# Performance work log

Measured on AMD Instinct MI355X. Metric: run time of the kernel, lower is better.

The kernel has to match this reference:

```python
import jax, jax.numpy as jnp
import numpy as np

N_NODES = 100000
N_EDGES = 3200000
IN_CH = 512
HID = 16
OUT_CH = 2


def setup_inputs() -> dict:
    key = jax.random.key(0)
    k1, k2, k3, k4 = jax.random.split(key, 4)
    x = jax.random.normal(k1, (N_NODES, IN_CH), dtype=jnp.float32)
    edge_index = jax.random.randint(k2, (2, N_EDGES), 0, N_NODES, dtype=jnp.int32)
    # GCNConv weight (glorot-style scale) and zero bias; Linear xavier weight, zero bias
    W1 = jax.random.normal(k3, (IN_CH, HID), dtype=jnp.float32) * np.float32(np.sqrt(2.0 / (IN_CH + HID)))
    b1 = jnp.zeros((HID,), dtype=jnp.float32)
    W2 = jax.random.normal(k4, (HID, OUT_CH), dtype=jnp.float32) * np.float32(np.sqrt(2.0 / (HID + OUT_CH)))
    b2 = jnp.zeros((OUT_CH,), dtype=jnp.float32)
    return {"x": x, "edge_index": edge_index, "W1": W1, "b1": b1, "W2": W2, "b2": b2}


def reference(x, edge_index, W1, b1, W2, b2):
    # GCNConv with default add_self_loops=True, normalize=True:
    #   out = D^{-1/2} (A + I) D^{-1/2} X W1 + b1, then Linear(16, out).
    n = x.shape[0]
    loops = jnp.arange(n, dtype=edge_index.dtype)
    row = jnp.concatenate([edge_index[0], loops])  # source nodes j
    col = jnp.concatenate([edge_index[1], loops])  # target nodes i
    deg = jax.ops.segment_sum(jnp.ones_like(col, dtype=x.dtype), col, num_segments=n)
    dinv = jnp.where(deg > 0, jax.lax.rsqrt(deg), jnp.zeros_like(deg))
    norm = dinv[row] * dinv[col]  # [E+N]
    xw = x @ W1  # [N, 16] project first (PyG GCNConv order)
    agg = jax.ops.segment_sum(xw[row] * norm[:, None], col, num_segments=n)  # scatter-add to targets
    h = agg + b1
    return h @ W2 + b2  # [N, out_channels]
```

## Files before the change

### kernel.cpp

```cpp
#include <hip/hip_runtime.h>


constexpr int N_NODES = 100000;
constexpr int N_EDGES = 3200000;
constexpr int IN_CH   = 512;
constexpr int HID     = 16;
constexpr int OUT_CH  = 2;

constexpr int NBUCK      = (N_NODES + 255) / 256;
constexpr int BIN_BLOCKS = 320;
constexpr int EPB        = N_EDGES / BIN_BLOCKS;
constexpr int XW_BLOCKS  = (N_NODES + 63) / 64;

typedef __attribute__((ext_vector_type(4))) float floatx4;


__global__ __launch_bounds__(1024) void k_count_wc(const int* __restrict__ tgt,
                                                   int* __restrict__ hist,
                                                   const float* __restrict__ W1,
                                                   const float* __restrict__ b1,
                                                   const float* __restrict__ W2,
                                                   const float* __restrict__ b2,
                                                   float* __restrict__ Wc,
                                                   float* __restrict__ bconst) {
    if (blockIdx.x == BIN_BLOCKS) {
        for (int i = threadIdx.x; i < IN_CH * OUT_CH; i += 1024) {
            int c = i >> 1, o = i & 1;
            float s = 0.f;
#pragma unroll
            for (int h = 0; h < HID; ++h) s += W1[c * HID + h] * W2[h * OUT_CH + o];
            Wc[i] = s;
        }
        if (threadIdx.x < OUT_CH) {
            float bo = b2[threadIdx.x];
#pragma unroll
            for (int h = 0; h < HID; ++h) bo += b1[h] * W2[h * OUT_CH + threadIdx.x];
            bconst[threadIdx.x] = bo;
        }
        return;
    }
    __shared__ int h[NBUCK];
    for (int i = threadIdx.x; i < NBUCK; i += 1024) h[i] = 0;
    __syncthreads();
    int e0 = blockIdx.x * EPB;
    for (int e = e0 + threadIdx.x; e < e0 + EPB; e += 1024)
        atomicAdd(&h[tgt[e] >> 8], 1);
    __syncthreads();
    for (int i = threadIdx.x; i < NBUCK; i += 1024)
        hist[blockIdx.x * NBUCK + i] = h[i];
}

__global__ __launch_bounds__(64) void k_colscan(int* __restrict__ hist,
                                                int* __restrict__ coltot) {
    int b = blockIdx.x;
    int lane = threadIdx.x;
    int v[5];
    int s = 0;
#pragma unroll
    for (int j = 0; j < 5; ++j) {
        v[j] = hist[(lane * 5 + j) * NBUCK + b];
        s += v[j];
    }
    int inc = s;
#pragma unroll
    for (int off = 1; off < 64; off <<= 1) {
        int n = __shfl_up(inc, off);
        if (lane >= off) inc += n;
    }
    int excl = inc - s;
#pragma unroll
    for (int j = 0; j < 5; ++j) {
        hist[(lane * 5 + j) * NBUCK + b] = excl;
        excl += v[j];
    }
    if (lane == 63) coltot[b] = inc;
}

__global__ __launch_bounds__(512) void k_basescan(const int* __restrict__ coltot,
                                                  int* __restrict__ bbase) {
    __shared__ int tmp[512];
    int tid = threadIdx.x;
    int v = (tid < NBUCK) ? coltot[tid] : 0;
    tmp[tid] = v;
    __syncthreads();
#pragma unroll
    for (int off = 1; off < 512; off <<= 1) {
        int tv = (tid >= off) ? tmp[tid - off] : 0;
        __syncthreads();
        tmp[tid] += tv;
        __syncthreads();
    }
    if (tid < NBUCK) bbase[tid] = tmp[tid] - v;
    if (tid == NBUCK - 1) bbase[NBUCK] = tmp[tid];
}

__global__ __launch_bounds__(1024) void k_bin_xw(const int* __restrict__ ei,
                                                 const int* __restrict__ hist,
                                                 const int* __restrict__ coltot,
                                                 const int* __restrict__ bbase,
                                                 int* __restrict__ binned,
                                                 const float* __restrict__ x,
                                                 const float* __restrict__ Wc,
                                                 float2* __restrict__ t2) {
    if (blockIdx.x < BIN_BLOCKS) {
        __shared__ int goff[NBUCK];
        __shared__ int rlen[NBUCK];
        __shared__ int lofs[512];
        __shared__ int lcur[NBUCK];
        __shared__ int stage[EPB];
        int blk = blockIdx.x;
        int tid = threadIdx.x;
        for (int b = tid; b < NBUCK; b += 1024) {
            int g  = hist[blk * NBUCK + b];
            int nx = (blk == BIN_BLOCKS - 1) ? coltot[b]
                                             : hist[(blk + 1) * NBUCK + b];
            goff[b] = g;
            rlen[b] = nx - g;
        }
        __syncthreads();
        if (tid < 512) lofs[tid] = (tid < NBUCK) ? rlen[tid] : 0;
        __syncthreads();
#pragma unroll
        for (int off = 1; off < 512; off <<= 1) {
            int tv = 0;
            if (tid < 512 && tid >= off) tv = lofs[tid - off];
            __syncthreads();
            if (tid < 512) lofs[tid] += tv;
            __syncthreads();
        }
        for (int b = tid; b < NBUCK; b += 1024)
            lcur[b] = lofs[b] - rlen[b];
        __syncthreads();
        int e0 = blk * EPB;
        for (int e = e0 + tid; e < e0 + EPB; e += 1024) {
            int tg = ei[N_EDGES + e];
            int b = tg >> 8;
            int lpos = atomicAdd(&lcur[b], 1);
            stage[lpos] = ((tg & 255) << 20) | ei[e];
        }
        __syncthreads();
        int wv = tid >> 6, lane = tid & 63;
        for (int b = wv; b < NBUCK; b += 16) {
            int len = rlen[b];
            int gbase = bbase[b] + goff[b];
            int lbase = lofs[b] - len;
            for (int i = lane; i < len; i += 64)
                binned[gbase + i] = stage[lbase + i];
        }
        return;
    }
    int nb = blockIdx.x - BIN_BLOCKS;
    int wv = threadIdx.x >> 6;
    int lane = threadIdx.x & 63;
    int node = nb * 64 + wv * 4;
    int r0 = min(node,     N_NODES - 1);
    int r1 = min(node + 1, N_NODES - 1);
    int r2 = min(node + 2, N_NODES - 1);
    int r3 = min(node + 3, N_NODES - 1);
    const floatx4* x0 = reinterpret_cast<const floatx4*>(x + (size_t)r0 * IN_CH + lane * 8);
    const floatx4* x1 = reinterpret_cast<const floatx4*>(x + (size_t)r1 * IN_CH + lane * 8);
    const floatx4* x2 = reinterpret_cast<const floatx4*>(x + (size_t)r2 * IN_CH + lane * 8);
    const floatx4* x3 = reinterpret_cast<const floatx4*>(x + (size_t)r3 * IN_CH + lane * 8);
    const floatx4* wr = reinterpret_cast<const floatx4*>(Wc + lane * 16);
    floatx4 a0 = x0[0], a1 = x0[1];
    floatx4 b0 = x1[0], b1 = x1[1];
    floatx4 c0 = x2[0], c1 = x2[1];
    floatx4 d0 = x3[0], d1 = x3[1];
    floatx4 w0 = wr[0], w1 = wr[1], w2 = wr[2], w3 = wr[3];
    float s0x = a0[0]*w0[0] + a0[1]*w0[2] + a0[2]*w1[0] + a0[3]*w1[2]
              + a1[0]*w2[0] + a1[1]*w2[2] + a1[2]*w3[0] + a1[3]*w3[2];
    float s0y = a0[0]*w0[1] + a0[1]*w0[3] + a0[2]*w1[1] + a0[3]*w1[3]
              + a1[0]*w2[1] + a1[1]*w2[3] + a1[2]*w3[1] + a1[3]*w3[3];
    float s1x = b0[0]*w0[0] + b0[1]*w0[2] + b0[2]*w1[0] + b0[3]*w1[2]
              + b1[0]*w2[0] + b1[1]*w2[2] + b1[2]*w3[0] + b1[3]*w3[2];
    float s1y = b0[0]*w0[1] + b0[1]*w0[3] + b0[2]*w1[1] + b0[3]*w1[3]
              + b1[0]*w2[1] + b1[1]*w2[3] + b1[2]*w3[1] + b1[3]*w3[3];
    float s2x = c0[0]*w0[0] + c0[1]*w0[2] + c0[2]*w1[0] + c0[3]*w1[2]
              + c1[0]*w2[0] + c1[1]*w2[2] + c1[2]*w3[0] + c1[3]*w3[2];
    float s2y = c0[0]*w0[1] + c0[1]*w0[3] + c0[2]*w1[1] + c0[3]*w1[3]
              + c1[0]*w2[1] + c1[1]*w2[3] + c1[2]*w3[1] + c1[3]*w3[3];
    float s3x = d0[0]*w0[0] + d0[1]*w0[2] + d0[2]*w1[0] + d0[3]*w1[2]
              + d1[0]*w2[0] + d1[1]*w2[2] + d1[2]*w3[0] + d1[3]*w3[2];
    float s3y = d0[0]*w0[1] + d0[1]*w0[3] + d0[2]*w1[1] + d0[3]*w1[3]
              + d1[0]*w2[1] + d1[1]*w2[3] + d1[2]*w3[1] + d1[3]*w3[3];
#pragma unroll
    for (int off = 32; off; off >>= 1) {
        s0x += __shfl_xor(s0x, off); s0y += __shfl_xor(s0y, off);
        s1x += __shfl_xor(s1x, off); s1y += __shfl_xor(s1y, off);
        s2x += __shfl_xor(s2x, off); s2y += __shfl_xor(s2y, off);
        s3x += __shfl_xor(s3x, off); s3y += __shfl_xor(s3y, off);
    }
    if (node + lane < N_NODES) {
        if      (lane == 0) t2[node]     = make_float2(s0x, s0y);
        else if (lane == 1) t2[node + 1] = make_float2(s1x, s1y);
        else if (lane == 2) t2[node + 2] = make_float2(s2x, s2y);
        else if (lane == 3) t2[node + 3] = make_float2(s3x, s3y);
    }
}

__global__ __launch_bounds__(1024) void k_dinv(const int* __restrict__ bbase,
                                               const int* __restrict__ binned,
                                               float* __restrict__ dinv,
                                               float2* __restrict__ t2) {
    __shared__ int cnt[256];
    if (threadIdx.x < 256) cnt[threadIdx.x] = 0;
    __syncthreads();
    int b = blockIdx.x;
    int s = bbase[b], e = bbase[b + 1];
    for (int i = s + threadIdx.x; i < e; i += 1024)
        atomicAdd(&cnt[binned[i] >> 20], 1);
    __syncthreads();
    if (threadIdx.x < 256) {
        int node = (b << 8) + threadIdx.x;
        if (node < N_NODES) {
            float di = rsqrtf((float)(cnt[threadIdx.x] + 1));
            dinv[node] = di;
            float2 v = t2[node];
            t2[node] = make_float2(v.x * di, v.y * di);
        }
    }
}

__global__ __launch_bounds__(1024) void k_acc(const int* __restrict__ bbase,
                                              const int* __restrict__ binned,
                                              const float2* __restrict__ t2,
                                              const float* __restrict__ dinv,
                                              const float* __restrict__ bconst,
                                              float2* __restrict__ out) {
    __shared__ float acc0[256];
    __shared__ float acc1[256];
    if (threadIdx.x < 256) {
        acc0[threadIdx.x] = 0.f;
        acc1[threadIdx.x] = 0.f;
    }
    __syncthreads();
    int b = blockIdx.x;
    int s = bbase[b], e = bbase[b + 1];
    for (int i = s + threadIdx.x; i < e; i += 1024) {
        int v = binned[i];
        float2 ts = t2[v & 0xFFFFF];
        atomicAdd(&acc0[v >> 20], ts.x);
        atomicAdd(&acc1[v >> 20], ts.y);
    }
    __syncthreads();
    if (threadIdx.x < 256) {
        int node = (b << 8) + threadIdx.x;
        if (node < N_NODES) {
            float2 self = t2[node];
            float di = dinv[node];
            out[node] = make_float2(di * (acc0[threadIdx.x] + self.x) + bconst[0],
                                    di * (acc1[threadIdx.x] + self.y) + bconst[1]);
        }
    }
}

extern "C" void kernel_launch(void* const* d_in, const int* in_sizes, int n_in,
                              void* d_out, int out_size, void* d_ws, size_t ws_size,
                              hipStream_t stream) {
    const float* x  = (const float*)d_in[0];
    const int*   ei = (const int*)d_in[1];
    const float* W1 = (const float*)d_in[2];
    const float* b1 = (const float*)d_in[3];
    const float* W2 = (const float*)d_in[4];
    const float* b2 = (const float*)d_in[5];

    char* ws = (char*)d_ws;
    int*    hist   = (int*)   (ws + 0);
    int*    coltot = (int*)   (ws + 500480);
    int*    bbase  = (int*)   (ws + 502048);
    float*  Wc     = (float*) (ws + 503616);
    float*  bconst = (float*) (ws + 507712);
    float*  dinv   = (float*) (ws + 507728);
    float2* t2     = (float2*)(ws + 907728);
    int*    binned = (int*)   (ws + 1707728);

    k_count_wc<<<BIN_BLOCKS + 1, 1024, 0, stream>>>(ei + N_EDGES, hist,
                                                    W1, b1, W2, b2, Wc, bconst);
    k_colscan <<<NBUCK, 64, 0, stream>>>(hist, coltot);
    k_basescan<<<1, 512, 0, stream>>>(coltot, bbase);
    k_bin_xw  <<<BIN_BLOCKS + XW_BLOCKS, 1024, 0, stream>>>(ei, hist, coltot,
                                                            bbase, binned,
                                                            x, Wc, t2);
    k_dinv    <<<NBUCK, 1024, 0, stream>>>(bbase, binned, dinv, t2);
    k_acc     <<<NBUCK, 1024, 0, stream>>>(bbase, binned, t2, dinv, bconst,
                                           (float2*)d_out);
}
```

Baseline: 371.4 us.

## Fuse all stages into one cooperative persistent kernel with grid syncs

Replaces the six separate kernel launches (count, column scan, base scan, bin+xw, dinv, accumulate) with a single cooperative kernel whose persistent blocks loop over virtual blocks and separate stages with grid.sync. The edge-count partitioning also changes from 320 to 512 virtual blocks, which shrinks the per-block staging buffer to fit a shared 8192-int scratch array, and the copy-out uses 16-lane groups instead of full wavefronts. The aim is to remove launch gaps and tail effects between stages. The cost is fixed grid size (at most 512 blocks, limited by occupancy), grid-wide barrier overhead, and larger per-block loops.

```diff
diff --git a/kernel.cpp b/kernel.cpp
--- a/kernel.cpp
+++ b/kernel.cpp
@@ -1,4 +1,7 @@
 #include <hip/hip_runtime.h>
+#include <hip/hip_cooperative_groups.h>
+
+namespace cg = cooperative_groups;
 
 
 constexpr int N_NODES = 100000;
@@ -7,258 +10,245 @@
 constexpr int HID     = 16;
 constexpr int OUT_CH  = 2;
 
-constexpr int NBUCK      = (N_NODES + 255) / 256;
-constexpr int BIN_BLOCKS = 320;
-constexpr int EPB        = N_EDGES / BIN_BLOCKS;
-constexpr int XW_BLOCKS  = (N_NODES + 63) / 64;
+constexpr int NBUCK  = (N_NODES + 255) / 256;
+constexpr int CNT_VB = 512;
+constexpr int EPB    = N_EDGES / CNT_VB;
+constexpr int XW_VB  = (N_NODES + 63) / 64;
 
 typedef __attribute__((ext_vector_type(4))) float floatx4;
 
 
-__global__ __launch_bounds__(1024) void k_count_wc(const int* __restrict__ tgt,
-                                                   int* __restrict__ hist,
-                                                   const float* __restrict__ W1,
-                                                   const float* __restrict__ b1,
-                                                   const float* __restrict__ W2,
-                                                   const float* __restrict__ b2,
-                                                   float* __restrict__ Wc,
-                                                   float* __restrict__ bconst) {
-    if (blockIdx.x == BIN_BLOCKS) {
-        for (int i = threadIdx.x; i < IN_CH * OUT_CH; i += 1024) {
+__global__ __launch_bounds__(1024) void k_mega(const int* __restrict__ ei,
+                                               const float* __restrict__ x,
+                                               const float* __restrict__ W1,
+                                               const float* __restrict__ b1,
+                                               const float* __restrict__ W2,
+                                               const float* __restrict__ b2,
+                                               int* __restrict__ hist,
+                                               int* __restrict__ coltot,
+                                               int* __restrict__ bbase,
+                                               float* __restrict__ Wc,
+                                               float* __restrict__ bconst,
+                                               float* __restrict__ dinv,
+                                               float2* __restrict__ t2,
+                                               int* __restrict__ binned,
+                                               float2* __restrict__ out) {
+    __shared__ int smem[8192];
+    cg::grid_group grid = cg::this_grid();
+    const int tid = threadIdx.x;
+    const int G = gridDim.x;
+    const int* tgt = ei + N_EDGES;
+
+    for (int v = blockIdx.x; v < CNT_VB; v += G) {
+        for (int i = tid; i < NBUCK; i += 1024) smem[i] = 0;
+        __syncthreads();
+        int e0 = v * EPB;
+        for (int e = e0 + tid; e < e0 + EPB; e += 1024)
+            atomicAdd(&smem[tgt[e] >> 8], 1);
+        __syncthreads();
+        for (int i = tid; i < NBUCK; i += 1024)
+            hist[v * NBUCK + i] = smem[i];
+        __syncthreads();
+    }
+    if (blockIdx.x == 0) {
+        for (int i = tid; i < IN_CH * OUT_CH; i += 1024) {
             int c = i >> 1, o = i & 1;
             float s = 0.f;
 #pragma unroll
             for (int h = 0; h < HID; ++h) s += W1[c * HID + h] * W2[h * OUT_CH + o];
             Wc[i] = s;
         }
-        if (threadIdx.x < OUT_CH) {
-            float bo = b2[threadIdx.x];
-#pragma unroll
-            for (int h = 0; h < HID; ++h) bo += b1[h] * W2[h * OUT_CH + threadIdx.x];
-            bconst[threadIdx.x] = bo;
-        }
-        return;
-    }
-    __shared__ int h[NBUCK];
-    for (int i = threadIdx.x; i < NBUCK; i += 1024) h[i] = 0;
-    __syncthreads();
-    int e0 = blockIdx.x * EPB;
-    for (int e = e0 + threadIdx.x; e < e0 + EPB; e += 1024)
-        atomicAdd(&h[tgt[e] >> 8], 1);
-    __syncthreads();
-    for (int i = threadIdx.x; i < NBUCK; i += 1024)
-        hist[blockIdx.x * NBUCK + i] = h[i];
-}
-
-__global__ __launch_bounds__(64) void k_colscan(int* __restrict__ hist,
-                                                int* __restrict__ coltot) {
-    int b = blockIdx.x;
-    int lane = threadIdx.x;
-    int v[5];
-    int s = 0;
-#pragma unroll
-    for (int j = 0; j < 5; ++j) {
-        v[j] = hist[(lane * 5 + j) * NBUCK + b];
-        s += v[j];
-    }
-    int inc = s;
-#pragma unroll
-    for (int off = 1; off < 64; off <<= 1) {
-        int n = __shfl_up(inc, off);
-        if (lane >= off) inc += n;
-    }
-    int excl = inc - s;
-#pragma unroll
-    for (int j = 0; j < 5; ++j) {
-        hist[(lane * 5 + j) * NBUCK + b] = excl;
-        excl += v[j];
-    }
-    if (lane == 63) coltot[b] = inc;
-}
-
-__global__ __launch_bounds__(512) void k_basescan(const int* __restrict__ coltot,
-                                                  int* __restrict__ bbase) {
-    __shared__ int tmp[512];
-    int tid = threadIdx.x;
-    int v = (tid < NBUCK) ? coltot[tid] : 0;
-    tmp[tid] = v;
-    __syncthreads();
-#pragma unroll
-    for (int off = 1; off < 512; off <<= 1) {
-        int tv = (tid >= off) ? tmp[tid - off] : 0;
-        __syncthreads();
-        tmp[tid] += tv;
-        __syncthreads();
-    }
-    if (tid < NBUCK) bbase[tid] = tmp[tid] - v;
-    if (tid == NBUCK - 1) bbase[NBUCK] = tmp[tid];
-}
-
-__global__ __launch_bounds__(1024) void k_bin_xw(const int* __restrict__ ei,
-                                                 const int* __restrict__ hist,
-                                                 const int* __restrict__ coltot,
-                                                 const int* __restrict__ bbase,
-                                                 int* __restrict__ binned,
-                                                 const float* __restrict__ x,
-                                                 const float* __restrict__ Wc,
-                                                 float2* __restrict__ t2) {
-    if (blockIdx.x < BIN_BLOCKS) {
-        __shared__ int goff[NBUCK];
-        __shared__ int rlen[NBUCK];
-        __shared__ int lofs[512];
-        __shared__ int lcur[NBUCK];
-        __shared__ int stage[EPB];
-        int blk = blockIdx.x;
-        int tid = threadIdx.x;
-        for (int b = tid; b < NBUCK; b += 1024) {
-            int g  = hist[blk * NBUCK + b];
-            int nx = (blk == BIN_BLOCKS - 1) ? coltot[b]
-                                             : hist[(blk + 1) * NBUCK + b];
-            goff[b] = g;
-            rlen[b] = nx - g;
-        }
-        __syncthreads();
-        if (tid < 512) lofs[tid] = (tid < NBUCK) ? rlen[tid] : 0;
+        if (tid < OUT_CH) {
+            float bo = b2[tid];
+#pragma unroll
+            for (int h = 0; h < HID; ++h) bo += b1[h] * W2[h * OUT_CH + tid];
+            bconst[tid] = bo;
+        }
+    }
+    grid.sync();
+
+    for (int b = blockIdx.x; b < NBUCK; b += G) {
+        int v = 0;
+        if (tid < CNT_VB) v = hist[tid * NBUCK + b];
+        if (tid < 512) smem[tid] = v;
         __syncthreads();
 #pragma unroll
         for (int off = 1; off < 512; off <<= 1) {
-            int tv = 0;
-            if (tid < 512 && tid >= off) tv = lofs[tid - off];
-            __syncthreads();
-            if (tid < 512) lofs[tid] += tv;
-            __syncthreads();
-        }
-        for (int b = tid; b < NBUCK; b += 1024)
-            lcur[b] = lofs[b] - rlen[b];
-        __syncthreads();
-        int e0 = blk * EPB;
-        for (int e = e0 + tid; e < e0 + EPB; e += 1024) {
-            int tg = ei[N_EDGES + e];
-            int b = tg >> 8;
-            int lpos = atomicAdd(&lcur[b], 1);
-            stage[lpos] = ((tg & 255) << 20) | ei[e];
-        }
-        __syncthreads();
-        int wv = tid >> 6, lane = tid & 63;
-        for (int b = wv; b < NBUCK; b += 16) {
-            int len = rlen[b];
-            int gbase = bbase[b] + goff[b];
-            int lbase = lofs[b] - len;
-            for (int i = lane; i < len; i += 64)
-                binned[gbase + i] = stage[lbase + i];
-        }
-        return;
-    }
-    int nb = blockIdx.x - BIN_BLOCKS;
-    int wv = threadIdx.x >> 6;
-    int lane = threadIdx.x & 63;
-    int node = nb * 64 + wv * 4;
-    int r0 = min(node,     N_NODES - 1);
-    int r1 = min(node + 1, N_NODES - 1);
-    int r2 = min(node + 2, N_NODES - 1);
-    int r3 = min(node + 3, N_NODES - 1);
-    const floatx4* x0 = reinterpret_cast<const floatx4*>(x + (size_t)r0 * IN_CH + lane * 8);
-    const floatx4* x1 = reinterpret_cast<const floatx4*>(x + (size_t)r1 * IN_CH + lane * 8);
-    const floatx4* x2 = reinterpret_cast<const floatx4*>(x + (size_t)r2 * IN_CH + lane * 8);
-    const floatx4* x3 = reinterpret_cast<const floatx4*>(x + (size_t)r3 * IN_CH + lane * 8);
-    const floatx4* wr = reinterpret_cast<const floatx4*>(Wc + lane * 16);
-    floatx4 a0 = x0[0], a1 = x0[1];
-    floatx4 b0 = x1[0], b1 = x1[1];
-    floatx4 c0 = x2[0], c1 = x2[1];
-    floatx4 d0 = x3[0], d1 = x3[1];
-    floatx4 w0 = wr[0], w1 = wr[1], w2 = wr[2], w3 = wr[3];
-    float s0x = a0[0]*w0[0] + a0[1]*w0[2] + a0[2]*w1[0] + a0[3]*w1[2]
-              + a1[0]*w2[0] + a1[1]*w2[2] + a1[2]*w3[0] + a1[3]*w3[2];
-    float s0y = a0[0]*w0[1] + a0[1]*w0[3] + a0[2]*w1[1] + a0[3]*w1[3]
-              + a1[0]*w2[1] + a1[1]*w2[3] + a1[2]*w3[1] + a1[3]*w3[3];
-    float s1x = b0[0]*w0[0] + b0[1]*w0[2] + b0[2]*w1[0] + b0[3]*w1[2]
-              + b1[0]*w2[0] + b1[1]*w2[2] + b1[2]*w3[0] + b1[3]*w3[2];
-    float s1y = b0[0]*w0[1] + b0[1]*w0[3] + b0[2]*w1[1] + b0[3]*w1[3]
-              + b1[0]*w2[1] + b1[1]*w2[3] + b1[2]*w3[1] + b1[3]*w3[3];
-    float s2x = c0[0]*w0[0] + c0[1]*w0[2] + c0[2]*w1[0] + c0[3]*w1[2]
-              + c1[0]*w2[0] + c1[1]*w2[2] + c1[2]*w3[0] + c1[3]*w3[2];
-    float s2y = c0[0]*w0[1] + c0[1]*w0[3] + c0[2]*w1[1] + c0[3]*w1[3]
-              + c1[0]*w2[1] + c1[1]*w2[3] + c1[2]*w3[1] + c1[3]*w3[3];
-    float s3x = d0[0]*w0[0] + d0[1]*w0[2] + d0[2]*w1[0] + d0[3]*w1[2]
-              + d1[0]*w2[0] + d1[1]*w2[2] + d1[2]*w3[0] + d1[3]*w3[2];
-    float s3y = d0[0]*w0[1] + d0[1]*w0[3] + d0[2]*w1[1] + d0[3]*w1[3]
-              + d1[0]*w2[1] + d1[1]*w2[3] + d1[2]*w3[1] + d1[3]*w3[3];
-#pragma unroll
-    for (int off = 32; off; off >>= 1) {
-        s0x += __shfl_xor(s0x, off); s0y += __shfl_xor(s0y, off);
-        s1x += __shfl_xor(s1x, off); s1y += __shfl_xor(s1y, off);
-        s2x += __shfl_xor(s2x, off); s2y += __shfl_xor(s2y, off);
-        s3x += __shfl_xor(s3x, off); s3y += __shfl_xor(s3y, off);
-    }
-    if (node + lane < N_NODES) {
-        if      (lane == 0) t2[node]     = make_float2(s0x, s0y);
-        else if (lane == 1) t2[node + 1] = make_float2(s1x, s1y);
-        else if (lane == 2) t2[node + 2] = make_float2(s2x, s2y);
-        else if (lane == 3) t2[node + 3] = make_float2(s3x, s3y);
-    }
-}
-
-__global__ __launch_bounds__(1024) void k_dinv(const int* __restrict__ bbase,
-                                               const int* __restrict__ binned,
-                                               float* __restrict__ dinv,
-                                               float2* __restrict__ t2) {
-    __shared__ int cnt[256];
-    if (threadIdx.x < 256) cnt[threadIdx.x] = 0;
-    __syncthreads();
-    int b = blockIdx.x;
-    int s = bbase[b], e = bbase[b + 1];
-    for (int i = s + threadIdx.x; i < e; i += 1024)
-        atomicAdd(&cnt[binned[i] >> 20], 1);
-    __syncthreads();
-    if (threadIdx.x < 256) {
-        int node = (b << 8) + threadIdx.x;
-        if (node < N_NODES) {
-            float di = rsqrtf((float)(cnt[threadIdx.x] + 1));
-            dinv[node] = di;
-            float2 v = t2[node];
-            t2[node] = make_float2(v.x * di, v.y * di);
-        }
-    }
-}
-
-__global__ __launch_bounds__(1024) void k_acc(const int* __restrict__ bbase,
-                                              const int* __restrict__ binned,
-                                              const float2* __restrict__ t2,
-                                              const float* __restrict__ dinv,
-                                              const float* __restrict__ bconst,
-                                              float2* __restrict__ out) {
-    __shared__ float acc0[256];
-    __shared__ float acc1[256];
-    if (threadIdx.x < 256) {
-        acc0[threadIdx.x] = 0.f;
-        acc1[threadIdx.x] = 0.f;
-    }
-    __syncthreads();
-    int b = blockIdx.x;
-    int s = bbase[b], e = bbase[b + 1];
-    for (int i = s + threadIdx.x; i < e; i += 1024) {
-        int v = binned[i];
-        float2 ts = t2[v & 0xFFFFF];
-        atomicAdd(&acc0[v >> 20], ts.x);
-        atomicAdd(&acc1[v >> 20], ts.y);
-    }
-    __syncthreads();
-    if (threadIdx.x < 256) {
-        int node = (b << 8) + threadIdx.x;
-        if (node < N_NODES) {
-            float2 self = t2[node];
-            float di = dinv[node];
-            out[node] = make_float2(di * (acc0[threadIdx.x] + self.x) + bconst[0],
-                                    di * (acc1[threadIdx.x] + self.y) + bconst[1]);
-        }
+            int tv = (tid < 512 && tid >= off) ? smem[tid - off] : 0;
+            __syncthreads();
+            if (tid < 512) smem[tid] += tv;
+            __syncthreads();
+        }
+        if (tid < CNT_VB) hist[tid * NBUCK + b] = smem[tid] - v;
+        if (tid == 511) coltot[b] = smem[511];
+        __syncthreads();
+    }
+    grid.sync();
+
+    if (blockIdx.x == 0) {
+        int v = 0;
+        if (tid < NBUCK) v = coltot[tid];
+        if (tid < 512) smem[tid] = v;
+        __syncthreads();
+#pragma unroll
+        for (int off = 1; off < 512; off <<= 1) {
+            int tv = (tid < 512 && tid >= off) ? smem[tid - off] : 0;
+            __syncthreads();
+            if (tid < 512) smem[tid] += tv;
+            __syncthreads();
+        }
+        if (tid < NBUCK) bbase[tid] = smem[tid] - v;
+        if (tid == NBUCK - 1) bbase[NBUCK] = smem[tid];
+    }
+    grid.sync();
+
+    for (int v = blockIdx.x; v < CNT_VB + XW_VB; v += G) {
+        if (v < CNT_VB) {
+            int* stage = smem;
+            int* goff  = smem + 6272;
+            int* rlen  = smem + 6720;
+            int* lcur  = smem + 7168;
+            int* lofs  = smem + 7616;
+            for (int b = tid; b < NBUCK; b += 1024) {
+                int g  = hist[v * NBUCK + b];
+                int nx = (v == CNT_VB - 1) ? coltot[b] : hist[(v + 1) * NBUCK + b];
+                goff[b] = g;
+                rlen[b] = nx - g;
+            }
+            __syncthreads();
+            if (tid < 512) lofs[tid] = (tid < NBUCK) ? rlen[tid] : 0;
+            __syncthreads();
+#pragma unroll
+            for (int off = 1; off < 512; off <<= 1) {
+                int tv = (tid < 512 && tid >= off) ? lofs[tid - off] : 0;
+                __syncthreads();
+                if (tid < 512) lofs[tid] += tv;
+                __syncthreads();
+            }
+            for (int b = tid; b < NBUCK; b += 1024)
+                lcur[b] = lofs[b] - rlen[b];
+            __syncthreads();
+            int e0 = v * EPB;
+            for (int e = e0 + tid; e < e0 + EPB; e += 1024) {
+                int tg = tgt[e];
+                int b = tg >> 8;
+                int lpos = atomicAdd(&lcur[b], 1);
+                stage[lpos] = ((tg & 255) << 20) | ei[e];
+            }
+            __syncthreads();
+            int grp = tid >> 4, li = tid & 15;
+            for (int b = grp; b < NBUCK; b += 64) {
+                int len = rlen[b];
+                int gbase = bbase[b] + goff[b];
+                int lbase = lofs[b] - len;
+                for (int i = li; i < len; i += 16)
+                    binned[gbase + i] = stage[lbase + i];
+            }
+            __syncthreads();
+        } else {
+            int nb = v - CNT_VB;
+            int wv = tid >> 6;
+            int lane = tid & 63;
+            int node = nb * 64 + wv * 4;
+            int r0 = min(node,     N_NODES - 1);
+            int r1 = min(node + 1, N_NODES - 1);
+            int r2 = min(node + 2, N_NODES - 1);
+            int r3 = min(node + 3, N_NODES - 1);
+            const floatx4* x0 = reinterpret_cast<const floatx4*>(x + (size_t)r0 * IN_CH + lane * 8);
+            const floatx4* x1 = reinterpret_cast<const floatx4*>(x + (size_t)r1 * IN_CH + lane * 8);
+            const floatx4* x2 = reinterpret_cast<const floatx4*>(x + (size_t)r2 * IN_CH + lane * 8);
+            const floatx4* x3 = reinterpret_cast<const floatx4*>(x + (size_t)r3 * IN_CH + lane * 8);
+            const floatx4* wr = reinterpret_cast<const floatx4*>(Wc + lane * 16);
+            floatx4 a0 = x0[0], a1 = x0[1];
+            floatx4 b0 = x1[0], b1v = x1[1];
+            floatx4 c0 = x2[0], c1 = x2[1];
+            floatx4 d0 = x3[0], d1 = x3[1];
+            floatx4 w0 = wr[0], w1 = wr[1], w2 = wr[2], w3 = wr[3];
+            float s0x = a0[0]*w0[0] + a0[1]*w0[2] + a0[2]*w1[0] + a0[3]*w1[2]
+                      + a1[0]*w2[0] + a1[1]*w2[2] + a1[2]*w3[0] + a1[3]*w3[2];
+            float s0y = a0[0]*w0[1] + a0[1]*w0[3] + a0[2]*w1[1] + a0[3]*w1[3]
+                      + a1[0]*w2[1] + a1[1]*w2[3] + a1[2]*w3[1] + a1[3]*w3[3];
+            float s1x = b0[0]*w0[0] + b0[1]*w0[2] + b0[2]*w1[0] + b0[3]*w1[2]
+                      + b1v[0]*w2[0] + b1v[1]*w2[2] + b1v[2]*w3[0] + b1v[3]*w3[2];
+            float s1y = b0[0]*w0[1] + b0[1]*w0[3] + b0[2]*w1[1] + b0[3]*w1[3]
+                      + b1v[0]*w2[1] + b1v[1]*w2[3] + b1v[2]*w3[1] + b1v[3]*w3[3];
+            float s2x = c0[0]*w0[0] + c0[1]*w0[2] + c0[2]*w1[0] + c0[3]*w1[2]
+                      + c1[0]*w2[0] + c1[1]*w2[2] + c1[2]*w3[0] + c1[3]*w3[2];
+            float s2y = c0[0]*w0[1] + c0[1]*w0[3] + c0[2]*w1[1] + c0[3]*w1[3]
+                      + c1[0]*w2[1] + c1[1]*w2[3] + c1[2]*w3[1] + c1[3]*w3[3];
+            float s3x = d0[0]*w0[0] + d0[1]*w0[2] + d0[2]*w1[0] + d0[3]*w1[2]
+                      + d1[0]*w2[0] + d1[1]*w2[2] + d1[2]*w3[0] + d1[3]*w3[2];
+            float s3y = d0[0]*w0[1] + d0[1]*w0[3] + d0[2]*w1[1] + d0[3]*w1[3]
+                      + d1[0]*w2[1] + d1[1]*w2[3] + d1[2]*w3[1] + d1[3]*w3[3];
+#pragma unroll
+            for (int off = 32; off; off >>= 1) {
+                s0x += __shfl_xor(s0x, off); s0y += __shfl_xor(s0y, off);
+                s1x += __shfl_xor(s1x, off); s1y += __shfl_xor(s1y, off);
+                s2x += __shfl_xor(s2x, off); s2y += __shfl_xor(s2y, off);
+                s3x += __shfl_xor(s3x, off); s3y += __shfl_xor(s3y, off);
+            }
+            if (node + lane < N_NODES) {
+                if      (lane == 0) t2[node]     = make_float2(s0x, s0y);
+                else if (lane == 1) t2[node + 1] = make_float2(s1x, s1y);
+                else if (lane == 2) t2[node + 2] = make_float2(s2x, s2y);
+                else if (lane == 3) t2[node + 3] = make_float2(s3x, s3y);
+            }
+        }
+    }
+    grid.sync();
+
+    for (int b = blockIdx.x; b < NBUCK; b += G) {
+        int* cnt = smem;
+        if (tid < 256) cnt[tid] = 0;
+        __syncthreads();
+        int s = bbase[b], e = bbase[b + 1];
+        for (int i = s + tid; i < e; i += 1024)
+            atomicAdd(&cnt[binned[i] >> 20], 1);
+        __syncthreads();
+        if (tid < 256) {
+            int node = (b << 8) + tid;
+            if (node < N_NODES) {
+                float di = rsqrtf((float)(cnt[tid] + 1));
+                dinv[node] = di;
+                float2 t = t2[node];
+                t2[node] = make_float2(t.x * di, t.y * di);
+            }
+        }
+        __syncthreads();
+    }
+    grid.sync();
+
+    for (int b = blockIdx.x; b < NBUCK; b += G) {
+        float* a0 = reinterpret_cast<float*>(smem);
+        float* a1 = a0 + 256;
+        if (tid < 256) { a0[tid] = 0.f; a1[tid] = 0.f; }
+        __syncthreads();
+        int s = bbase[b], e = bbase[b + 1];
+        for (int i = s + tid; i < e; i += 1024) {
+            int vv = binned[i];
+            float2 ts = t2[vv & 0xFFFFF];
+            atomicAdd(&a0[vv >> 20], ts.x);
+            atomicAdd(&a1[vv >> 20], ts.y);
+        }
+        __syncthreads();
+        if (tid < 256) {
+            int node = (b << 8) + tid;
+            if (node < N_NODES) {
+                float2 self = t2[node];
+                float di = dinv[node];
+                out[node] = make_float2(di * (a0[tid] + self.x) + bconst[0],
+                                        di * (a1[tid] + self.y) + bconst[1]);
+            }
+        }
+        __syncthreads();
     }
 }
 
 extern "C" void kernel_launch(void* const* d_in, const int* in_sizes, int n_in,
                               void* d_out, int out_size, void* d_ws, size_t ws_size,
                               hipStream_t stream) {
+    const int*   ei = (const int*)d_in[1];
     const float* x  = (const float*)d_in[0];
-    const int*   ei = (const int*)d_in[1];
     const float* W1 = (const float*)d_in[2];
     const float* b1 = (const float*)d_in[3];
     const float* W2 = (const float*)d_in[4];
@@ -266,22 +256,28 @@
 
     char* ws = (char*)d_ws;
     int*    hist   = (int*)   (ws + 0);
-    int*    coltot = (int*)   (ws + 500480);
-    int*    bbase  = (int*)   (ws + 502048);
-    float*  Wc     = (float*) (ws + 503616);
-    float*  bconst = (float*) (ws + 507712);
-    float*  dinv   = (float*) (ws + 507728);
-    float2* t2     = (float2*)(ws + 907728);
-    int*    binned = (int*)   (ws + 1707728);
-
-    k_count_wc<<<BIN_BLOCKS + 1, 1024, 0, stream>>>(ei + N_EDGES, hist,
-                                                    W1, b1, W2, b2, Wc, bconst);
-    k_colscan <<<NBUCK, 64, 0, stream>>>(hist, coltot);
-    k_basescan<<<1, 512, 0, stream>>>(coltot, bbase);
-    k_bin_xw  <<<BIN_BLOCKS + XW_BLOCKS, 1024, 0, stream>>>(ei, hist, coltot,
-                                                            bbase, binned,
-                                                            x, Wc, t2);
-    k_dinv    <<<NBUCK, 1024, 0, stream>>>(bbase, binned, dinv, t2);
-    k_acc     <<<NBUCK, 1024, 0, stream>>>(bbase, binned, t2, dinv, bconst,
-                                           (float2*)d_out);
+    int*    coltot = (int*)   (ws + 800768);
+    int*    bbase  = (int*)   (ws + 802336);
+    float*  Wc     = (float*) (ws + 803904);
+    float*  bconst = (float*) (ws + 808000);
+    float*  dinv   = (float*) (ws + 808016);
+    float2* t2     = (float2*)(ws + 1208016);
+    int*    binned = (int*)   (ws + 2008016);
+    float2* outp   = (float2*)d_out;
+
+    static int occ = -1;
+    if (occ < 0) {
+        if (hipOccupancyMaxActiveBlocksPerMultiprocessor(&occ, k_mega, 1024, 0)
+                != hipSuccess || occ < 1)
+            occ = 1;
+    }
+    int G = occ * 256;
+    if (G > 512) G = 512;
+
+    void* args[] = {(void*)&ei, (void*)&x, (void*)&W1, (void*)&b1,
+                    (void*)&W2, (void*)&b2, (void*)&hist, (void*)&coltot,
+                    (void*)&bbase, (void*)&Wc, (void*)&bconst, (void*)&dinv,
+                    (void*)&t2, (void*)&binned, (void*)&outp};
+    hipLaunchCooperativeKernel((void*)k_mega, dim3(G), dim3(1024), args, 0,
+                               stream);
 }
```

New measurement: 547.9 us. 47.5% more time.
